# Optimization experiments

Measured on AMD Instinct MI355X. Metric: run time of the kernel, lower is better.

## Reference

```python
import jax, jax.numpy as jnp
import numpy as np

B, S, D = 2, 2048, 1024
H = 16
DH = D // H  # 64


def setup_inputs() -> dict:
    key = jax.random.key(0)
    k1, k2, k3 = jax.random.split(key, 3)
    x = jax.random.normal(k1, (B, S, D), dtype=jnp.float32)
    W_qkv = jax.random.normal(k2, (D, 3 * D), dtype=jnp.float32) * 0.01
    b_qkv = jnp.zeros((3 * D,), dtype=jnp.float32)
    W_out = jax.random.normal(k3, (D, D), dtype=jnp.float32) * 0.01
    b_out = jnp.zeros((D,), dtype=jnp.float32)
    return {"x": x, "W_qkv": W_qkv, "b_qkv": b_qkv, "W_out": W_out, "b_out": b_out}


def reference(x, W_qkv, b_qkv, W_out, b_out):
    b, s, d = x.shape
    h, dh = H, DH
    # fused QKV projection
    qkv = x @ W_qkv + b_qkv                       # [b, s, 3d]
    qkv = qkv.reshape(b, s, 3, h, dh)
    q, k, v = qkv[:, :, 0], qkv[:, :, 1], qkv[:, :, 2]  # [b, s, h, dh]
    q = q.transpose(0, 2, 1, 3)                    # [b, h, s, dh]
    k = k.transpose(0, 2, 1, 3)
    v = v.transpose(0, 2, 1, 3)
    inv_sqrt_d = jnp.asarray(1.0 / np.sqrt(dh), dtype=x.dtype)
    scores = jnp.einsum('bhqd,bhkd->bhqk', q, k) * inv_sqrt_d  # [b, h, s, s]
    causal = jnp.tril(jnp.ones((s, s), dtype=bool))[None, None]
    # source masks with -10000.0 (not -inf)
    scores = jnp.where(causal, scores, jnp.asarray(-10000.0, dtype=scores.dtype))
    probs = jax.nn.softmax(scores, axis=-1)
    attn = jnp.einsum('bhqk,bhkd->bhqd', probs, v)  # [b, h, s, dh]
    attn = attn.transpose(0, 2, 1, 3).reshape(b, s, d)
    return attn @ W_out + b_out
```

## Files before the change

kernel.cpp:

```cpp
#include <hip/hip_runtime.h>
#include <hip/hip_bf16.h>

#define B_  2
#define S_  2048
#define D_  1024
#define H_  16
#define DH_ 64
#define M_  (B_ * S_)
#define QKV_LD (3 * D_)

typedef __bf16 bf16x8 __attribute__((ext_vector_type(8)));
typedef float  f32x4  __attribute__((ext_vector_type(4)));
typedef unsigned short us4 __attribute__((ext_vector_type(4)));
typedef unsigned short us8 __attribute__((ext_vector_type(8)));

__device__ inline unsigned short f2bf(float f) {
  union { __bf16 h; unsigned short u; } cv; cv.h = (__bf16)f; return cv.u;
}
__device__ inline float bf2f(unsigned short u) {
  union { unsigned int i; float f; } cv; cv.i = ((unsigned int)u) << 16; return cv.f;
}
__device__ inline unsigned int pk2bf(float lo, float hi) {
  return (unsigned int)f2bf(lo) | ((unsigned int)f2bf(hi) << 16);
}
__device__ inline void cstore(float* p, float v) { *p = v; }
__device__ inline void cstore(unsigned short* p, float v) { *p = f2bf(v); }

__device__ inline void gload_lds16(const void* g, void* lds) {
  __builtin_amdgcn_global_load_lds(
      (const __attribute__((address_space(1))) unsigned int*)g,
      (__attribute__((address_space(3))) unsigned int*)lds, 16, 0, 0);
}

__global__ __launch_bounds__(256) void conv_bf16(const float* __restrict__ in,
                                                 unsigned short* __restrict__ out, int n4) {
  int i = blockIdx.x * 256 + threadIdx.x;
  if (i >= n4) return;
  float4 v = ((const float4*)in)[i];
  us4 p = { f2bf(v.x), f2bf(v.y), f2bf(v.z), f2bf(v.w) };
  ((us4*)out)[i] = p;
}

__global__ __launch_bounds__(256) void transpose_bf16(const float* __restrict__ W,
                                                      unsigned short* __restrict__ Wt,
                                                      int K, int N) {
  __shared__ float tile[32][33];
  const int t = threadIdx.x, tx = t & 31, ty = t >> 5;
  const int c0 = blockIdx.x * 32, r0 = blockIdx.y * 32;
  #pragma unroll
  for (int i = 0; i < 4; ++i)
    tile[ty + 8 * i][tx] = W[(size_t)(r0 + ty + 8 * i) * N + c0 + tx];
  __syncthreads();
  #pragma unroll
  for (int i = 0; i < 4; ++i)
    Wt[(size_t)(c0 + ty + 8 * i) * K + r0 + tx] = f2bf(tile[tx][ty + 8 * i]);
}

template<typename CT>
__global__ __launch_bounds__(256) void gemm_bf16_tn(
    const unsigned short* __restrict__ A,
    const unsigned short* __restrict__ Bt,
    const float* __restrict__ bias,
    CT* __restrict__ C, int N, int K) {
  __shared__ __align__(16) unsigned short smA[128 * 32];
  __shared__ __align__(16) unsigned short smB[128 * 32];
  const int t = threadIdx.x;
  const int w = t >> 6, l = t & 63;
  const int lg = l >> 4, lr = l & 15;
  const int row0 = blockIdx.y * 128, col0 = blockIdx.x * 128;
  const int wm = (w >> 1) * 64, wn = (w & 1) * 64;

  f32x4 acc[4][4] = {};

  for (int k0 = 0; k0 < K; k0 += 32) {
    __syncthreads();
    #pragma unroll
    for (int i = 0; i < 2; ++i) {
      const int inst = 2 * w + i;
      const int r = inst * 16 + (l >> 2);
      const int cb = (l & 3) * 8;
      gload_lds16(A  + (size_t)(row0 + r) * K + k0 + cb, &smA[inst * 512]);
      gload_lds16(Bt + (size_t)(col0 + r) * K + k0 + cb, &smB[inst * 512]);
    }
    __syncthreads();

    bf16x8 af[4], bfr[4];
    #pragma unroll
    for (int m = 0; m < 4; ++m)
      af[m] = *(const bf16x8*)&smA[(wm + m * 16 + lr) * 32 + lg * 8];
    #pragma unroll
    for (int n = 0; n < 4; ++n)
      bfr[n] = *(const bf16x8*)&smB[(wn + n * 16 + lr) * 32 + lg * 8];
    #pragma unroll
    for (int m = 0; m < 4; ++m)
      #pragma unroll
      for (int n = 0; n < 4; ++n)
        acc[m][n] = __builtin_amdgcn_mfma_f32_16x16x32_bf16(af[m], bfr[n], acc[m][n], 0, 0, 0);
  }

  #pragma unroll
  for (int m = 0; m < 4; ++m) {
    #pragma unroll
    for (int n = 0; n < 4; ++n) {
      const int col = col0 + wn + n * 16 + lr;
      const float bv = bias[col];
      #pragma unroll
      for (int r = 0; r < 4; ++r) {
        const int row = row0 + wm + m * 16 + lg * 4 + r;
        cstore(&C[(size_t)row * N + col], acc[m][n][r] + bv);
      }
    }
  }
}

__global__ __launch_bounds__(256) void attn_fwd_mfma(
    const unsigned short* __restrict__ qkv, unsigned short* __restrict__ attn_out) {
  const int bid = blockIdx.x + gridDim.x * blockIdx.y;
  const int xcd = bid & 7;
  const int li  = bid >> 3;
  const int bh  = xcd * 4 + (li >> 4);
  const int x   = li & 15;
  const int b = bh / H_, h = bh % H_;
  const unsigned short* base = qkv + (size_t)b * S_ * QKV_LD;

  __shared__ __align__(16) char smK[2][64 * 128];
  __shared__ __align__(16) char smV[2][64 * 128];

  const int t  = threadIdx.x;
  const int w  = t >> 6;
  const int l  = t & 63;
  const int lg = l >> 4;
  const int lr = l & 15;

  const unsigned short* kbase = base + D_ + h * DH_;
  const unsigned short* vbase = base + 2 * D_ + h * DH_;

  us8 kreg[2], vreg[2];
  const int kp  = (t & 31) * 2;
  const int vdb = (t >> 5) * 8;

  auto issue_loads = [&](int k0) {
    #pragma unroll
    for (int it = 0; it < 2; ++it) {
      int idx = t + it * 256;
      int r = idx >> 3, c = idx & 7;
      kreg[it] = *(const us8*)(kbase + (size_t)(k0 + r) * QKV_LD + c * 8);
    }
    vreg[0] = *(const us8*)(vbase + (size_t)(k0 + kp) * QKV_LD + vdb);
    vreg[1] = *(const us8*)(vbase + (size_t)(k0 + kp + 1) * QKV_LD + vdb);
  };
  auto write_lds = [&](int buf) {
    #pragma unroll
    for (int it = 0; it < 2; ++it) {
      int idx = t + it * 256;
      int r = idx >> 3, c = idx & 7;
      *(us8*)(smK[buf] + r * 128 + ((c * 16) ^ ((r & 7) << 4))) = kreg[it];
    }
    #pragma unroll
    for (int j = 0; j < 8; ++j) {
      int row = vdb + j;
      unsigned int pv = (unsigned int)vreg[0][j] | ((unsigned int)vreg[1][j] << 16);
      *(unsigned int*)(smV[buf] + row * 128 + ((2 * kp) ^ ((row & 7) << 4))) = pv;
    }
  };

  #pragma unroll 1
  for (int sel = 0; sel < 2; ++sel) {
    const int qt = sel ? (31 - x) : x;
    const int q0 = qt * 64;
    const int qw0 = q0 + w * 16;

    bf16x8 qf[2];
    {
      const unsigned short* qp = base + (size_t)(qw0 + lr) * QKV_LD + h * DH_ + 8 * lg;
      #pragma unroll
      for (int ks = 0; ks < 2; ++ks) {
        us8 qv = *(const us8*)(qp + 32 * ks);
        #pragma unroll
        for (int e = 0; e < 8; ++e) qf[ks][e] = (__bf16)(bf2f(qv[e]) * 0.125f);
      }
    }

    float mrun = -1e30f, lrun = 0.f;
    f32x4 acc_o[4] = {};

    const int ntiles = qt + 1;
    issue_loads(0);
    write_lds(0);
    __syncthreads();

    for (int kti = 0; kti < ntiles; ++kti) {
      const int k0 = kti * 64;
      const int cur = kti & 1;

      if (kti + 1 < ntiles) issue_loads((kti + 1) * 64);

      if (k0 <= qw0 + 15) {
        f32x4 sc[4] = {};
        #pragma unroll
        for (int kt = 0; kt < 4; ++kt)
          #pragma unroll
          for (int ks = 0; ks < 2; ++ks) {
            int row = kt * 16 + lr;
            bf16x8 kb_ = *(const bf16x8*)(smK[cur] + row * 128 +
                                          (((ks * 64) + 16 * lg) ^ ((row & 7) << 4)));
            sc[kt] = __builtin_amdgcn_mfma_f32_16x16x32_bf16(kb_, qf[ks], sc[kt], 0, 0, 0);
          }

        if (k0 + 63 > qw0) {
          #pragma unroll
          for (int kt = 0; kt < 4; ++kt)
            #pragma unroll
            for (int r = 0; r < 4; ++r) {
              int kc = k0 + kt * 16 + lg * 4 + r;
              if (kc > qw0 + lr) sc[kt][r] = -1e30f;
            }
        }

        float v = sc[0][0];
        #pragma unroll
        for (int kt = 0; kt < 4; ++kt)
          #pragma unroll
          for (int r = 0; r < 4; ++r) v = fmaxf(v, sc[kt][r]);
        v = fmaxf(v, __shfl_xor(v, 16));
        v = fmaxf(v, __shfl_xor(v, 32));
        const float mnew = fmaxf(mrun, v);
        const float alpha = __expf(mrun - mnew);
        mrun = mnew;
        float s = 0.f;
        #pragma unroll
        for (int kt = 0; kt < 4; ++kt)
          #pragma unroll
          for (int r = 0; r < 4; ++r) {
            float p = __expf(sc[kt][r] - mnew);
            sc[kt][r] = p;
            s += p;
          }
        s += __shfl_xor(s, 16);
        s += __shfl_xor(s, 32);
        lrun = lrun * alpha + s;

        unsigned int P2[4][2];
        #pragma unroll
        for (int kt = 0; kt < 4; ++kt)
          #pragma unroll
          for (int j = 0; j < 2; ++j)
            P2[kt][j] = pk2bf(sc[kt][2 * j], sc[kt][2 * j + 1]);

        union { unsigned int u[4]; bf16x8 v8; } pa[2];
        #pragma unroll
        for (int ks = 0; ks < 2; ++ks)
          #pragma unroll
          for (int q2 = 0; q2 < 4; ++q2) {
            int src = 16 * (2 * (lg & 1) + (q2 >> 1)) + lr;
            unsigned int a = __shfl(P2[2 * ks][q2 & 1], src);
            unsigned int bsel = __shfl(P2[2 * ks + 1][q2 & 1], src);
            pa[ks].u[q2] = (lg & 2) ? bsel : a;
          }

        float alphaO[4];
        #pragma unroll
        for (int r = 0; r < 4; ++r)
          alphaO[r] = __shfl(alpha, (l & 48) | (lg * 4 + r));
        #pragma unroll
        for (int dt = 0; dt < 4; ++dt)
          #pragma unroll
          for (int r = 0; r < 4; ++r) acc_o[dt][r] *= alphaO[r];

        #pragma unroll
        for (int dt = 0; dt < 4; ++dt)
          #pragma unroll
          for (int ks = 0; ks < 2; ++ks) {
            int row = dt * 16 + lr;
            bf16x8 vb = *(const bf16x8*)(smV[cur] + row * 128 +
                                         (((ks * 64) + 16 * lg) ^ ((row & 7) << 4)));
            acc_o[dt] = __builtin_amdgcn_mfma_f32_16x16x32_bf16(pa[ks].v8, vb, acc_o[dt], 0, 0, 0);
          }
      }

      if (kti + 1 < ntiles) write_lds(cur ^ 1);
      __syncthreads();
    }

    const float inv = 1.0f / lrun;
    float invO[4];
    #pragma unroll
    for (int r = 0; r < 4; ++r)
      invO[r] = __shfl(inv, (l & 48) | (lg * 4 + r));
    #pragma unroll
    for (int dt = 0; dt < 4; ++dt)
      #pragma unroll
      for (int r = 0; r < 4; ++r)
        attn_out[(size_t)(b * S_ + qw0 + lg * 4 + r) * D_ + h * DH_ + dt * 16 + lr] =
            f2bf(acc_o[dt][r] * invO[r]);
  }
}

extern "C" void kernel_launch(void* const* d_in, const int* in_sizes, int n_in,
                              void* d_out, int out_size, void* d_ws, size_t ws_size,
                              hipStream_t stream) {
  const float* x     = (const float*)d_in[0];
  const float* W_qkv = (const float*)d_in[1];
  const float* b_qkv = (const float*)d_in[2];
  const float* W_out = (const float*)d_in[3];
  const float* b_out = (const float*)d_in[4];
  float* out = (float*)d_out;

  char* ws = (char*)d_ws;
  unsigned short* qkv_bf  = (unsigned short*)ws;  ws += (size_t)M_ * QKV_LD * 2;
  unsigned short* attn_bf = (unsigned short*)ws;  ws += (size_t)M_ * D_ * 2;
  unsigned short* x_bf    = (unsigned short*)ws;  ws += (size_t)M_ * D_ * 2;
  unsigned short* wqkvT   = (unsigned short*)ws;  ws += (size_t)QKV_LD * D_ * 2;
  unsigned short* woutT   = (unsigned short*)ws;

  dim3 blk(256);
  conv_bf16<<<(M_ * D_ / 4 + 255) / 256, blk, 0, stream>>>(x, x_bf, M_ * D_ / 4);
  transpose_bf16<<<dim3(QKV_LD / 32, D_ / 32), blk, 0, stream>>>(W_qkv, wqkvT, D_, QKV_LD);
  transpose_bf16<<<dim3(D_ / 32, D_ / 32), blk, 0, stream>>>(W_out, woutT, D_, D_);
  gemm_bf16_tn<unsigned short><<<dim3(QKV_LD / 128, M_ / 128), blk, 0, stream>>>(
      x_bf, wqkvT, b_qkv, qkv_bf, QKV_LD, D_);
  attn_fwd_mfma<<<dim3(S_ / 64 / 2, B_ * H_), blk, 0, stream>>>(qkv_bf, attn_bf);
  gemm_bf16_tn<float><<<dim3(D_ / 128, M_ / 128), blk, 0, stream>>>(
      attn_bf, woutT, b_out, out, D_, D_);
}
```

Baseline: 138.9 us.

## Merge prep kernels, permute K rows to drop P shuffles, add lazy rescale with exp2

The three preprocessing launches (x conversion and two weight transposes) are merged into one kernel indexed by a flat block id, saving launch overhead. In attention, K rows are permuted in LDS so the score MFMA output already matches the A-operand layout for the PV MFMA, which removes the cross-lane shuffles used to rebuild P. Q is prescaled by log2(e)/sqrt(d) so the kernel can use exp2f. The running max and output rescale are now skipped unless the new max exceeds the old one by more than 8, which leaves exponent headroom but changes rounding slightly.

```diff
diff --git a/kernel.cpp b/kernel.cpp
--- a/kernel.cpp
+++ b/kernel.cpp
@@ -32,21 +32,26 @@
       (__attribute__((address_space(3))) unsigned int*)lds, 16, 0, 0);
 }
 
-__global__ __launch_bounds__(256) void conv_bf16(const float* __restrict__ in,
-                                                 unsigned short* __restrict__ out, int n4) {
-  int i = blockIdx.x * 256 + threadIdx.x;
-  if (i >= n4) return;
-  float4 v = ((const float4*)in)[i];
-  us4 p = { f2bf(v.x), f2bf(v.y), f2bf(v.z), f2bf(v.w) };
-  ((us4*)out)[i] = p;
-}
-
-__global__ __launch_bounds__(256) void transpose_bf16(const float* __restrict__ W,
-                                                      unsigned short* __restrict__ Wt,
-                                                      int K, int N) {
+__global__ __launch_bounds__(256) void prep_all(
+    const float* __restrict__ x, unsigned short* __restrict__ x_bf,
+    const float* __restrict__ W_qkv, unsigned short* __restrict__ wqkvT,
+    const float* __restrict__ W_out, unsigned short* __restrict__ woutT) {
   __shared__ float tile[32][33];
-  const int t = threadIdx.x, tx = t & 31, ty = t >> 5;
-  const int c0 = blockIdx.x * 32, r0 = blockIdx.y * 32;
+  const int blk = blockIdx.x;
+  const int t = threadIdx.x;
+  if (blk < 4096) {
+    int i = blk * 256 + t;
+    float4 v = ((const float4*)x)[i];
+    us4 p = { f2bf(v.x), f2bf(v.y), f2bf(v.z), f2bf(v.w) };
+    ((us4*)x_bf)[i] = p;
+    return;
+  }
+  const float* W; unsigned short* Wt; int K, N, bi;
+  if (blk < 4096 + 3072) { bi = blk - 4096; W = W_qkv; Wt = wqkvT; K = D_; N = QKV_LD; }
+  else                   { bi = blk - 7168; W = W_out; Wt = woutT; K = D_; N = D_; }
+  const int bx = bi % (N / 32), by = bi / (N / 32);
+  const int tx = t & 31, ty = t >> 5;
+  const int c0 = bx * 32, r0 = by * 32;
   #pragma unroll
   for (int i = 0; i < 4; ++i)
     tile[ty + 8 * i][tx] = W[(size_t)(r0 + ty + 8 * i) * N + c0 + tx];
@@ -154,7 +159,8 @@
     for (int it = 0; it < 2; ++it) {
       int idx = t + it * 256;
       int r = idx >> 3, c = idx & 7;
-      *(us8*)(smK[buf] + r * 128 + ((c * 16) ^ ((r & 7) << 4))) = kreg[it];
+      int rho = (r & 0x23) | ((r & 0x04) << 2) | ((r & 0x18) >> 1);
+      *(us8*)(smK[buf] + rho * 128 + ((c * 16) ^ ((rho & 7) << 4))) = kreg[it];
     }
     #pragma unroll
     for (int j = 0; j < 8; ++j) {
@@ -177,7 +183,7 @@
       for (int ks = 0; ks < 2; ++ks) {
         us8 qv = *(const us8*)(qp + 32 * ks);
         #pragma unroll
-        for (int e = 0; e < 8; ++e) qf[ks][e] = (__bf16)(bf2f(qv[e]) * 0.125f);
+        for (int e = 0; e < 8; ++e) qf[ks][e] = (__bf16)(bf2f(qv[e]) * 0.18033688f);
       }
     }
 
@@ -212,60 +218,52 @@
           for (int kt = 0; kt < 4; ++kt)
             #pragma unroll
             for (int r = 0; r < 4; ++r) {
-              int kc = k0 + kt * 16 + lg * 4 + r;
+              int kc = k0 + ((kt >> 1) << 5) + (lg << 3) + ((kt & 1) << 2) + r;
               if (kc > qw0 + lr) sc[kt][r] = -1e30f;
             }
         }
 
-        float v = sc[0][0];
-        #pragma unroll
-        for (int kt = 0; kt < 4; ++kt)
-          #pragma unroll
-          for (int r = 0; r < 4; ++r) v = fmaxf(v, sc[kt][r]);
+        float v = fmaxf(fmaxf(sc[0][0], sc[0][1]), fmaxf(sc[0][2], sc[0][3]));
+        #pragma unroll
+        for (int kt = 1; kt < 4; ++kt)
+          v = fmaxf(v, fmaxf(fmaxf(sc[kt][0], sc[kt][1]), fmaxf(sc[kt][2], sc[kt][3])));
         v = fmaxf(v, __shfl_xor(v, 16));
         v = fmaxf(v, __shfl_xor(v, 32));
-        const float mnew = fmaxf(mrun, v);
-        const float alpha = __expf(mrun - mnew);
-        mrun = mnew;
+        if (!__all(v <= mrun + 8.0f)) {
+          const float mnew = fmaxf(mrun, v);
+          const float alpha = exp2f(mrun - mnew);
+          mrun = mnew;
+          float alphaO[4];
+          #pragma unroll
+          for (int r = 0; r < 4; ++r)
+            alphaO[r] = __shfl(alpha, (l & 48) | (lg * 4 + r));
+          #pragma unroll
+          for (int dt = 0; dt < 4; ++dt)
+            #pragma unroll
+            for (int r = 0; r < 4; ++r) acc_o[dt][r] *= alphaO[r];
+          lrun *= alpha;
+        }
         float s = 0.f;
         #pragma unroll
         for (int kt = 0; kt < 4; ++kt)
           #pragma unroll
           for (int r = 0; r < 4; ++r) {
-            float p = __expf(sc[kt][r] - mnew);
+            float p = exp2f(sc[kt][r] - mrun);
             sc[kt][r] = p;
             s += p;
           }
         s += __shfl_xor(s, 16);
         s += __shfl_xor(s, 32);
-        lrun = lrun * alpha + s;
-
-        unsigned int P2[4][2];
-        #pragma unroll
-        for (int kt = 0; kt < 4; ++kt)
-          #pragma unroll
-          for (int j = 0; j < 2; ++j)
-            P2[kt][j] = pk2bf(sc[kt][2 * j], sc[kt][2 * j + 1]);
+        lrun += s;
 
         union { unsigned int u[4]; bf16x8 v8; } pa[2];
         #pragma unroll
-        for (int ks = 0; ks < 2; ++ks)
-          #pragma unroll
-          for (int q2 = 0; q2 < 4; ++q2) {
-            int src = 16 * (2 * (lg & 1) + (q2 >> 1)) + lr;
-            unsigned int a = __shfl(P2[2 * ks][q2 & 1], src);
-            unsigned int bsel = __shfl(P2[2 * ks + 1][q2 & 1], src);
-            pa[ks].u[q2] = (lg & 2) ? bsel : a;
-          }
-
-        float alphaO[4];
-        #pragma unroll
-        for (int r = 0; r < 4; ++r)
-          alphaO[r] = __shfl(alpha, (l & 48) | (lg * 4 + r));
-        #pragma unroll
-        for (int dt = 0; dt < 4; ++dt)
-          #pragma unroll
-          for (int r = 0; r < 4; ++r) acc_o[dt][r] *= alphaO[r];
+        for (int ks = 0; ks < 2; ++ks) {
+          pa[ks].u[0] = pk2bf(sc[2 * ks][0], sc[2 * ks][1]);
+          pa[ks].u[1] = pk2bf(sc[2 * ks][2], sc[2 * ks][3]);
+          pa[ks].u[2] = pk2bf(sc[2 * ks + 1][0], sc[2 * ks + 1][1]);
+          pa[ks].u[3] = pk2bf(sc[2 * ks + 1][2], sc[2 * ks + 1][3]);
+        }
 
         #pragma unroll
         for (int dt = 0; dt < 4; ++dt)
@@ -314,9 +312,7 @@
   unsigned short* woutT   = (unsigned short*)ws;
 
   dim3 blk(256);
-  conv_bf16<<<(M_ * D_ / 4 + 255) / 256, blk, 0, stream>>>(x, x_bf, M_ * D_ / 4);
-  transpose_bf16<<<dim3(QKV_LD / 32, D_ / 32), blk, 0, stream>>>(W_qkv, wqkvT, D_, QKV_LD);
-  transpose_bf16<<<dim3(D_ / 32, D_ / 32), blk, 0, stream>>>(W_out, woutT, D_, D_);
+  prep_all<<<4096 + 3072 + 1024, blk, 0, stream>>>(x, x_bf, W_qkv, wqkvT, W_out, woutT);
   gemm_bf16_tn<unsigned short><<<dim3(QKV_LD / 128, M_ / 128), blk, 0, stream>>>(
       x_bf, wqkvT, b_qkv, qkv_bf, QKV_LD, D_);
   attn_fwd_mfma<<<dim3(S_ / 64 / 2, B_ * H_), blk, 0, stream>>>(qkv_bf, attn_bf);
```

Result: faster. 127.7 us (-8.0%).
